# Performance work log

Hardware: AMD Instinct MI355X
Metric: run time of the kernel (lower is better)

## Reference

```python
import jax, jax.numpy as jnp
import numpy as np

N, CAMS = 1, 4
C1, C2, NH = 256, 256, 8
H1, H2, W2 = 128, 64, 400
H, W = 128, 128


def setup_inputs() -> dict:
    key = jax.random.key(0)
    ks = jax.random.split(key, 16)
    sc = 0.02
    th = jax.random.uniform(ks[3], (N, CAMS)) * 2.0 * np.pi
    c, s = jnp.cos(th), jnp.sin(th)
    z, o = jnp.zeros_like(c), jnp.ones_like(c)
    rots = jnp.stack([jnp.stack([c, -s, z], -1), jnp.stack([s, c, z], -1), jnp.stack([z, z, o], -1)], -2)
    return {
        "list_a": jax.random.normal(ks[0], (N, C1, H, W), jnp.float32),
        "list_b": jax.random.normal(ks[1], (N * CAMS, C2, H2, W2), jnp.float32),
        "fov_list": jax.random.uniform(ks[2], (N, CAMS)) * 0.5 + 1.0,
        "rots_list": rots.astype(jnp.float32),
        "trans_list": jax.random.normal(ks[4], (N, CAMS, 3), jnp.float32),
        "fxs": jax.random.uniform(ks[5], (N, CAMS)) * 100.0 + 500.0,
        "cxs": jax.random.uniform(ks[6], (N, CAMS)) * 20.0 + 390.0,
        "pos_a": jax.random.normal(ks[7], (1, H1, C1), jnp.float32),
        "pos_b": jax.random.normal(ks[8], (1, H2, C2), jnp.float32),
        "Wq": jax.random.normal(ks[9], (C1, C1), jnp.float32) * sc,
        "bq": jnp.zeros((C1,), jnp.float32),
        "Wk": jax.random.normal(ks[10], (C1, C2), jnp.float32) * sc,
        "bk": jnp.zeros((C1,), jnp.float32),
        "Wv": jax.random.normal(ks[11], (C1, C2), jnp.float32) * sc,
        "bv": jnp.zeros((C1,), jnp.float32),
        "in_w": jax.random.normal(ks[12], (3 * C1, C1), jnp.float32) * sc,
        "in_b": jnp.zeros((3 * C1,), jnp.float32),
        "out_w": jax.random.normal(ks[13], (C1, C1), jnp.float32) * sc,
        "out_b": jnp.zeros((C1,), jnp.float32),
    }


def _polar_coords(w1, h1, Hh, Ww, rots, fx, cx):
    # per-pixel viewing angles from intrinsics (original image width hard-coded 800)
    pi = jnp.arange(w1, dtype=jnp.float32)
    pw = 800.0 / w1
    ang = jnp.arctan((pi * pw + pw / 2.0 - cx) / fx)
    R90 = jnp.array([[0.0, 1.0], [-1.0, 0.0]], jnp.float32)
    rot = R90 @ rots[:2, :2].astype(jnp.float32)
    cr, sr = rot[0, 0], rot[1, 0]
    ca = cr * jnp.cos(ang) + sr * jnp.sin(ang)
    sa = -sr * jnp.cos(ang) + cr * jnp.sin(ang)
    cxp = jnp.float32(Ww // 2)
    cyp = jnp.float32(Hh // 2)
    rmax = jnp.sqrt(cxp ** 2 + cyp ** 2)
    radii = jnp.linspace(0.0, 1.0, h1).reshape(h1, 1) * rmax
    x = cxp + radii * ca  # [h1, w1]
    y = cyp - radii * sa
    return x, y


def _bilinear(img, x, y):
    # img [C,H,W]; x,y pixel coords [h1,w1]; grid_sample(align_corners=True) after clamping
    Hh, Ww = img.shape[1], img.shape[2]
    x = jnp.clip(x, 0.0, Ww - 1.0)
    y = jnp.clip(y, 0.0, Hh - 1.0)
    x0 = jnp.floor(x); y0 = jnp.floor(y)
    x1 = jnp.clip(x0 + 1.0, 0.0, Ww - 1.0)
    y1 = jnp.clip(y0 + 1.0, 0.0, Hh - 1.0)
    wx = x - x0; wy = y - y0
    x0i, x1i = x0.astype(jnp.int32), x1.astype(jnp.int32)
    y0i, y1i = y0.astype(jnp.int32), y1.astype(jnp.int32)
    v00 = img[:, y0i, x0i]; v01 = img[:, y0i, x1i]
    v10 = img[:, y1i, x0i]; v11 = img[:, y1i, x1i]
    return v00 * (1 - wx) * (1 - wy) + v01 * wx * (1 - wy) + v10 * (1 - wx) * wy + v11 * wx * wy


def _mha(q, k, v, in_w, in_b, out_w, out_b, nh):
    E = q.shape[-1]
    dh = E // nh
    qq = q @ in_w[:E].T + in_b[:E]
    kk = k @ in_w[E:2 * E].T + in_b[E:2 * E]
    vv = v @ in_w[2 * E:].T + in_b[2 * E:]
    B, Lq, _ = q.shape
    Lk = k.shape[1]
    qq = qq.reshape(B, Lq, nh, dh)
    kk = kk.reshape(B, Lk, nh, dh)
    vv = vv.reshape(B, Lk, nh, dh)
    att = jnp.einsum('bqhd,bkhd->bhqk', qq, kk) / jnp.sqrt(jnp.float32(dh))
    p = jax.nn.softmax(att, axis=-1)
    o = jnp.einsum('bhqk,bkhd->bqhd', p, vv).reshape(B, Lq, E)
    return o @ out_w.T + out_b


def _forward(list_a, list_b, rots_list, fxs, cxs, pos_a, pos_b,
             Wq, bq, Wk, bk, Wv, bv, in_w, in_b, out_w, out_b):
    outs = []
    for i in range(list_a.shape[0]):
        a = list_a[i]
        C1_, h1, Wb = a.shape
        Hb = h1
        enh = None
        for j in (0, 3):  # cameras 1 and 2 are skipped by the original `continue`
            b = list_b[i * CAMS + j]
            C2_, h2, w2 = b.shape
            x, y = _polar_coords(w2, h1, a.shape[1], a.shape[2], rots_list[i, j], fxs[i, j], cxs[i, j])
            a_rect = _bilinear(a, x, y)                     # [C1, h1, w2]
            a_seq = jnp.transpose(a_rect, (2, 1, 0)) + pos_a  # [w2, h1, C1]
            b_seq = jnp.transpose(b, (2, 1, 0)) + pos_b       # [w2, h2, C2]
            q = a_seq @ Wq.T + bq
            k = b_seq @ Wk.T + bk
            v = b_seq @ Wv.T + bv
            o = _mha(q, k, v, in_w, in_b, out_w, out_b, NH)
            a_enh = jnp.transpose(o, (2, 1, 0))              # [C1, h1, w2]
            # scatter-add restore with nearest-pixel indices
            xi = jnp.clip(jnp.round(x), 0, a.shape[2] - 1).astype(jnp.int32)
            yi = jnp.clip(jnp.round(y), 0, a.shape[1] - 1).astype(jnp.int32)
            idx = (yi * a.shape[2] + xi).reshape(-1)
            vals = a_enh.reshape(C1_, -1)
            rest = jnp.zeros((C1_, a.shape[1] * a.shape[2]), a.dtype).at[:, idx].add(vals)
            cnt = jnp.zeros((a.shape[1] * a.shape[2],), a.dtype).at[idx].add(1.0)
            cnt = jnp.where(cnt == 0, 1.0, cnt)
            enh = (rest / cnt).reshape(a.shape)
            a = a + enh
        outs.append(a + enh)  # original double-adds the last camera's enhancement
    return jnp.stack(outs)


def reference(list_a, list_b, fov_list, rots_list, trans_list, fxs, cxs, pos_a, pos_b,
              Wq, bq, Wk, bk, Wv, bv, in_w, in_b, out_w, out_b):
    # fov_list / trans_list are accepted but unused in the original math path
    return _forward(list_a, list_b, rots_list, fxs, cxs, pos_a, pos_b,
                    Wq, bq, Wk, bk, Wv, bv, in_w, in_b, out_w, out_b)
```

## Files before the change

kernel.cpp:

```cpp
#include <hip/hip_runtime.h>

#define PIX 16384
#define MS 51200
#define MB 25600

typedef __attribute__((ext_vector_type(8))) short short8;
typedef __attribute__((ext_vector_type(4))) float floatx4;

__device__ inline ushort f2b(float x) {
  uint u = __float_as_uint(x);
  return (ushort)((u + 0x7fffu + ((u >> 16) & 1u)) >> 16);
}
__device__ inline float b2f(ushort u) {
  return __uint_as_float(((uint)u) << 16);
}

__global__ __launch_bounds__(256) void coords_kernel(
    const float* __restrict__ rots, const float* __restrict__ fxs,
    const float* __restrict__ cxs,
    float* __restrict__ xarr, float* __restrict__ yarr,
    int* __restrict__ idxarr, float* __restrict__ cnt)
{
  int jz = blockIdx.y;
  int j = jz ? 3 : 0;
  int s = blockIdx.x * 256 + threadIdx.x;
  int h = s / 400;
  int w = s - h * 400;
  float fx = fxs[j], cx = cxs[j];
  const float* R = rots + j * 9;
  float cr = R[3];
  float sr = -R[0];
  float t = (2.0f * (float)w + 1.0f - cx) / fx;
  float inv = 1.0f / sqrtf(1.0f + t * t);
  float ca = (cr + sr * t) * inv;
  float sa = (cr * t - sr) * inv;
  float rad = ((float)h * (1.0f / 127.0f)) * 90.50966799187808f;
  float x = 64.0f + rad * ca;
  float y = 64.0f - rad * sa;
  xarr[jz * MS + s] = x;
  yarr[jz * MS + s] = y;
  int xi = (int)fminf(fmaxf(rintf(x), 0.0f), 127.0f);
  int yi = (int)fminf(fmaxf(rintf(y), 0.0f), 127.0f);
  int pix = yi * 128 + xi;
  idxarr[jz * MS + s] = pix;
  atomicAdd(&cnt[jz * PIX + pix], 1.0f);
}

__global__ __launch_bounds__(256) void prefix_kernel(
    const float* __restrict__ cntg, int* __restrict__ offsetsg)
{
  const float* cnt = cntg + blockIdx.x * PIX;
  int* offsets = offsetsg + blockIdx.x * PIX;
  __shared__ int sh[256];
  int t = threadIdx.x;
  int base = t * 64;
  const float4* cp = (const float4*)(cnt + base);
  int sum = 0;
#pragma unroll
  for (int i = 0; i < 16; ++i) {
    float4 v = cp[i];
    sum += (int)v.x + (int)v.y + (int)v.z + (int)v.w;
  }
  sh[t] = sum;
  __syncthreads();
  for (int d = 1; d < 256; d <<= 1) {
    int v = (t >= d) ? sh[t - d] : 0;
    __syncthreads();
    sh[t] += v;
    __syncthreads();
  }
  int run = sh[t] - sum;
  int4* op = (int4*)(offsets + base);
#pragma unroll
  for (int i = 0; i < 16; ++i) {
    float4 v = cp[i];
    int a0 = (int)v.x, a1 = (int)v.y, a2 = (int)v.z, a3 = (int)v.w;
    int4 o;
    o.x = run; o.y = run + a0; o.z = run + a0 + a1; o.w = run + a0 + a1 + a2;
    op[i] = o;
    run += a0 + a1 + a2 + a3;
  }
}

__global__ __launch_bounds__(256) void fill_kernel(
    const int* __restrict__ idxarr, const int* __restrict__ offsets,
    int* __restrict__ cursor, int* __restrict__ order, int* __restrict__ pixs)
{
  int jz = blockIdx.y;
  int s = blockIdx.x * 256 + threadIdx.x;
  int pix = idxarr[jz * MS + s];
  int pos = offsets[jz * PIX + pix] + atomicAdd(&cursor[jz * PIX + pix], 1);
  order[jz * MS + pos] = (s % 400) * 128 + (s / 400);
  pixs[jz * MS + pos] = pix;
}

__global__ __launch_bounds__(256) void transpose_kernel(
    const float* __restrict__ src, ushort* __restrict__ dst)
{
  __shared__ float tile[64][65];
  int p0 = blockIdx.x * 64;
  int c0 = blockIdx.y * 64;
  int t = threadIdx.x;
  int pr = (t & 15) * 4;
  int cr = t >> 4;
#pragma unroll
  for (int q = 0; q < 4; ++q) {
    int c = cr + q * 16;
    float4 v = *(const float4*)(src + (size_t)(c0 + c) * PIX + p0 + pr);
    tile[pr + 0][c] = v.x;
    tile[pr + 1][c] = v.y;
    tile[pr + 2][c] = v.z;
    tile[pr + 3][c] = v.w;
  }
  __syncthreads();
  int p = t >> 2;
  int ch = (t & 3) * 16;
  ushort tmp[16];
#pragma unroll
  for (int i = 0; i < 16; ++i) tmp[i] = f2b(tile[p][ch + i]);
  ushort* d = dst + (size_t)(p0 + p) * 256 + c0 + ch;
  *(uint4*)(d) = *(uint4*)tmp;
  *(uint4*)(d + 8) = *(uint4*)(tmp + 8);
}

__global__ __launch_bounds__(256) void misc_kernel(
    const float* __restrict__ out_w, ushort* __restrict__ out_wh,
    const float* __restrict__ in_w, const float* __restrict__ in_b,
    const float* __restrict__ bq, const float* __restrict__ bk,
    const float* __restrict__ bv, float* __restrict__ beff)
{
  if (blockIdx.x < 64) {
    int t = blockIdx.x * 256 + threadIdx.x;
    float4 v = ((const float4*)out_w)[t];
    ushort4 o;
    o.x = f2b(v.x); o.y = f2b(v.y); o.z = f2b(v.z); o.w = f2b(v.w);
    ((ushort4*)out_wh)[t] = o;
  } else {
    int z = blockIdx.x - 64;
    int f = threadIdx.x;
    const float* bsrc = (z == 0) ? bq : ((z == 1) ? bk : bv);
    const float* row = in_w + (size_t)(z * 256 + f) * 256;
    float acc = in_b[z * 256 + f];
    for (int e = 0; e < 256; ++e) acc += row[e] * bsrc[e];
    beff[z * 256 + f] = acc;
  }
}

#define LFP 264
__device__ __forceinline__ void sampleproj_body(
    ushort* lf, int bx,
    const ushort* __restrict__ aT, const float* __restrict__ xarr,
    const float* __restrict__ yarr, const ushort* __restrict__ Wh,
    const float* __restrict__ bias, ushort* __restrict__ qh)
{
  int s0 = bx * 64;
  int tid = threadIdx.x;
  int lane = tid & 63;
  int wave = tid >> 6;
  int col = lane & 15, quad = lane >> 4;
  int c0 = lane * 4;

#pragma unroll 4
  for (int i = 0; i < 16; ++i) {
    int sl = wave * 16 + i;
    int s = s0 + sl;
    float x = fminf(fmaxf(xarr[s], 0.0f), 127.0f);
    float y = fminf(fmaxf(yarr[s], 0.0f), 127.0f);
    float x0f = floorf(x), y0f = floorf(y);
    int x0 = (int)x0f, y0 = (int)y0f;
    int x1 = min(x0 + 1, 127), y1 = min(y0 + 1, 127);
    float wx = x - x0f, wy = y - y0f;
    float w00 = (1.0f - wx) * (1.0f - wy);
    float w01 = wx * (1.0f - wy);
    float w10 = (1.0f - wx) * wy;
    float w11 = wx * wy;
    ushort4 v00 = *(const ushort4*)(aT + (size_t)(y0 * 128 + x0) * 256 + c0);
    ushort4 v01 = *(const ushort4*)(aT + (size_t)(y0 * 128 + x1) * 256 + c0);
    ushort4 v10 = *(const ushort4*)(aT + (size_t)(y1 * 128 + x0) * 256 + c0);
    ushort4 v11 = *(const ushort4*)(aT + (size_t)(y1 * 128 + x1) * 256 + c0);
    ushort4 o;
    o.x = f2b(w00 * b2f(v00.x) + w01 * b2f(v01.x) + w10 * b2f(v10.x) + w11 * b2f(v11.x));
    o.y = f2b(w00 * b2f(v00.y) + w01 * b2f(v01.y) + w10 * b2f(v10.y) + w11 * b2f(v11.y));
    o.z = f2b(w00 * b2f(v00.z) + w01 * b2f(v01.z) + w10 * b2f(v10.z) + w11 * b2f(v11.z));
    o.w = f2b(w00 * b2f(v00.w) + w01 * b2f(v01.w) + w10 * b2f(v10.w) + w11 * b2f(v11.w));
    *(ushort4*)&lf[sl * LFP + c0] = o;
  }
  __syncthreads();

  int fw = wave * 64;
  floatx4 acc[4][4];
#pragma unroll
  for (int i = 0; i < 4; ++i)
#pragma unroll
    for (int jx = 0; jx < 4; ++jx) acc[i][jx] = (floatx4){0.f, 0.f, 0.f, 0.f};

  for (int kb = 0; kb < 256; kb += 32) {
    short8 aop[4], bop[4];
#pragma unroll
    for (int tf = 0; tf < 4; ++tf)
      aop[tf] = *(const short8*)(Wh + (size_t)(fw + tf * 16 + col) * 256 + kb + quad * 8);
#pragma unroll
    for (int ts = 0; ts < 4; ++ts)
      bop[ts] = *(const short8*)&lf[(ts * 16 + col) * LFP + kb + quad * 8];
#pragma unroll
    for (int ts = 0; ts < 4; ++ts)
#pragma unroll
      for (int tf = 0; tf < 4; ++tf)
        acc[ts][tf] = __builtin_amdgcn_mfma_f32_16x16x32_bf16(
            aop[tf], bop[ts], acc[ts][tf], 0, 0, 0);
  }
#pragma unroll
  for (int ts = 0; ts < 4; ++ts) {
    int s = s0 + ts * 16 + col;
    int h = s / 400;
    int w = s - h * 400;
    size_t obase = (size_t)(w * 128 + h) * 256;
#pragma unroll
    for (int tf = 0; tf < 4; ++tf) {
      int f = fw + tf * 16 + quad * 4;
      float4 bv = *(const float4*)(bias + h * 256 + f);
      ushort4 ov;
      ov.x = f2b(acc[ts][tf][0] + bv.x);
      ov.y = f2b(acc[ts][tf][1] + bv.y);
      ov.z = f2b(acc[ts][tf][2] + bv.z);
      ov.w = f2b(acc[ts][tf][3] + bv.w);
      *(ushort4*)(qh + obase + f) = ov;
    }
  }
}

__device__ __forceinline__ void projKV_body(
    ushort* lb, int bx,
    const float* __restrict__ bsrc,
    const ushort* __restrict__ WhK, const ushort* __restrict__ WhV,
    const float* __restrict__ biasK, const float* __restrict__ biasV,
    ushort* __restrict__ kh, ushort* __restrict__ vh)
{
  int m0 = bx * 64;
  int tid = threadIdx.x;
  int lane = tid & 63;
  int wave = tid >> 6;
  int col = lane & 15, quad = lane >> 4;
  int fw = wave * 64;

  int pr = (tid & 15) * 4;
  int cb = tid >> 4;
#pragma unroll 4
  for (int q = 0; q < 16; ++q) {
    int c = cb + q * 16;
    float4 v = *(const float4*)(bsrc + (size_t)c * MB + m0 + pr);
    lb[(pr + 0) * LFP + c] = f2b(v.x);
    lb[(pr + 1) * LFP + c] = f2b(v.y);
    lb[(pr + 2) * LFP + c] = f2b(v.z);
    lb[(pr + 3) * LFP + c] = f2b(v.w);
  }
  __syncthreads();

  for (int z = 0; z < 2; ++z) {
    const ushort* Wh = z ? WhV : WhK;
    const float* bias = z ? biasV : biasK;
    ushort* out = z ? vh : kh;
    floatx4 acc[4][4];
#pragma unroll
    for (int i = 0; i < 4; ++i)
#pragma unroll
      for (int jx = 0; jx < 4; ++jx) acc[i][jx] = (floatx4){0.f, 0.f, 0.f, 0.f};

    for (int kb = 0; kb < 256; kb += 32) {
      short8 bop[4], aop[4];
#pragma unroll
      for (int ts = 0; ts < 4; ++ts)
        bop[ts] = *(const short8*)&lb[(ts * 16 + col) * LFP + kb + quad * 8];
#pragma unroll
      for (int tf = 0; tf < 4; ++tf)
        aop[tf] = *(const short8*)(Wh + (size_t)(fw + tf * 16 + col) * 256 + kb + quad * 8);
#pragma unroll
      for (int ts = 0; ts < 4; ++ts)
#pragma unroll
        for (int tf = 0; tf < 4; ++tf)
          acc[ts][tf] = __builtin_amdgcn_mfma_f32_16x16x32_bf16(
              aop[tf], bop[ts], acc[ts][tf], 0, 0, 0);
    }
#pragma unroll
    for (int ts = 0; ts < 4; ++ts) {
      int m = m0 + ts * 16 + col;
      int h = m / 400;
      int w = m - h * 400;
      size_t obase = (size_t)(w * 64 + h) * 256;
#pragma unroll
      for (int tf = 0; tf < 4; ++tf) {
        int f = fw + tf * 16 + quad * 4;
        float4 bv = *(const float4*)(bias + h * 256 + f);
        ushort4 ov;
        ov.x = f2b(acc[ts][tf][0] + bv.x);
        ov.y = f2b(acc[ts][tf][1] + bv.y);
        ov.z = f2b(acc[ts][tf][2] + bv.z);
        ov.w = f2b(acc[ts][tf][3] + bv.w);
        *(ushort4*)(out + obase + f) = ov;
      }
    }
  }
}

__global__ __launch_bounds__(256, 3) void proj_kernel(
    const ushort* __restrict__ aT, const float* __restrict__ xarr,
    const float* __restrict__ yarr, const ushort* __restrict__ weffh,
    const float* __restrict__ qpos, ushort* __restrict__ qh,
    const float* __restrict__ bsrc,
    const float* __restrict__ kpos, const float* __restrict__ vpos,
    ushort* __restrict__ kh, ushort* __restrict__ vh)
{
  __shared__ ushort lf[64 * LFP];
  if (blockIdx.x < 400)
    projKV_body(lf, blockIdx.x, bsrc, weffh + 65536, weffh + 131072,
                kpos, vpos, kh, vh);
  else
    sampleproj_body(lf, blockIdx.x - 400, aT, xarr, yarr, weffh, qpos, qh);
}

#define VP 72
#define PP 72
__global__ __launch_bounds__(256) void attn_mfma_kernel(
    const ushort* __restrict__ qh, const ushort* __restrict__ kh,
    const ushort* __restrict__ vh, ushort* __restrict__ obuf)
{
  __shared__ ushort lV[4][32 * VP];
  __shared__ ushort lP[4][16 * PP];
  int b = blockIdx.x;
  int hg = blockIdx.y & 1;
  int qb = blockIdx.y >> 1;
  int wave = threadIdx.x >> 6;
  int lane = threadIdx.x & 63;
  int head = hg * 4 + wave;
  int col = lane & 15, quad = lane >> 4;
  ushort* Vw = lV[wave];
  ushort* Pw = lP[wave];

  short8 bk0 = *(const short8*)(kh + ((size_t)(b * 64 +  0 + col)) * 256 + head * 32 + quad * 8);
  short8 bk1 = *(const short8*)(kh + ((size_t)(b * 64 + 16 + col)) * 256 + head * 32 + quad * 8);
  short8 bk2 = *(const short8*)(kh + ((size_t)(b * 64 + 32 + col)) * 256 + head * 32 + quad * 8);
  short8 bk3 = *(const short8*)(kh + ((size_t)(b * 64 + 48 + col)) * 256 + head * 32 + quad * 8);

  {
    const ushort* vsrc = vh + ((size_t)(b * 64 + lane)) * 256 + head * 32;
    ushort vr[32];
    *(uint4*)(vr) = *(const uint4*)(vsrc);
    *(uint4*)(vr + 8) = *(const uint4*)(vsrc + 8);
    *(uint4*)(vr + 16) = *(const uint4*)(vsrc + 16);
    *(uint4*)(vr + 24) = *(const uint4*)(vsrc + 24);
#pragma unroll
    for (int d = 0; d < 32; ++d) Vw[d * VP + lane] = vr[d];
  }
  short8 vA0 = *(const short8*)(Vw + (col) * VP + 0 * 32 + quad * 8);
  short8 vB0 = *(const short8*)(Vw + (16 + col) * VP + 0 * 32 + quad * 8);
  short8 vA1 = *(const short8*)(Vw + (col) * VP + 1 * 32 + quad * 8);
  short8 vB1 = *(const short8*)(Vw + (16 + col) * VP + 1 * 32 + quad * 8);

  const float scl = 0.17677669529663687f;
  for (int qt = qb * 4; qt < qb * 4 + 4; ++qt) {
    short8 aq = *(const short8*)(qh +
        ((size_t)(b * 128 + qt * 16 + col)) * 256 + head * 32 + quad * 8);
    floatx4 s0 = {0.f,0.f,0.f,0.f}, s1 = s0, s2 = s0, s3 = s0;
    s0 = __builtin_amdgcn_mfma_f32_16x16x32_bf16(aq, bk0, s0, 0, 0, 0);
    s1 = __builtin_amdgcn_mfma_f32_16x16x32_bf16(aq, bk1, s1, 0, 0, 0);
    s2 = __builtin_amdgcn_mfma_f32_16x16x32_bf16(aq, bk2, s2, 0, 0, 0);
    s3 = __builtin_amdgcn_mfma_f32_16x16x32_bf16(aq, bk3, s3, 0, 0, 0);
    float e[4][4], mr[4], sm[4];
#pragma unroll
    for (int r = 0; r < 4; ++r) {
      float v0 = s0[r] * scl, v1 = s1[r] * scl;
      float v2 = s2[r] * scl, v3 = s3[r] * scl;
      e[0][r] = v0; e[1][r] = v1; e[2][r] = v2; e[3][r] = v3;
      mr[r] = fmaxf(fmaxf(v0, v1), fmaxf(v2, v3));
    }
#pragma unroll
    for (int mask = 1; mask <= 8; mask <<= 1)
#pragma unroll
      for (int r = 0; r < 4; ++r)
        mr[r] = fmaxf(mr[r], __shfl_xor(mr[r], mask, 64));
#pragma unroll
    for (int r = 0; r < 4; ++r) {
      float acc = 0.f;
#pragma unroll
      for (int t = 0; t < 4; ++t) {
        float ev = __expf(e[t][r] - mr[r]);
        e[t][r] = ev;
        acc += ev;
      }
      sm[r] = acc;
    }
#pragma unroll
    for (int mask = 1; mask <= 8; mask <<= 1)
#pragma unroll
      for (int r = 0; r < 4; ++r)
        sm[r] += __shfl_xor(sm[r], mask, 64);
#pragma unroll
    for (int t = 0; t < 4; ++t)
#pragma unroll
      for (int r = 0; r < 4; ++r)
        Pw[(quad * 4 + r) * PP + t * 16 + col] = f2b(e[t][r]);
    floatx4 o0 = {0.f,0.f,0.f,0.f}, o1 = o0;
    {
      short8 ap0 = *(const short8*)(Pw + col * PP + 0 * 32 + quad * 8);
      o0 = __builtin_amdgcn_mfma_f32_16x16x32_bf16(ap0, vA0, o0, 0, 0, 0);
      o1 = __builtin_amdgcn_mfma_f32_16x16x32_bf16(ap0, vB0, o1, 0, 0, 0);
      short8 ap1 = *(const short8*)(Pw + col * PP + 1 * 32 + quad * 8);
      o0 = __builtin_amdgcn_mfma_f32_16x16x32_bf16(ap1, vA1, o0, 0, 0, 0);
      o1 = __builtin_amdgcn_mfma_f32_16x16x32_bf16(ap1, vB1, o1, 0, 0, 0);
    }
#pragma unroll
    for (int r = 0; r < 4; ++r) {
      float iv = 1.0f / sm[r];
      Pw[(quad * 4 + r) * PP + col] = f2b(o0[r] * iv);
      Pw[(quad * 4 + r) * PP + 16 + col] = f2b(o1[r] * iv);
    }
    int orow = lane >> 2, ochunk = lane & 3;
    uint4 ov = *(const uint4*)(Pw + orow * PP + ochunk * 8);
    *(uint4*)(obuf + (size_t)(b * 128 + qt * 16 + orow) * 256 + head * 32 + ochunk * 8) = ov;
  }
}

__global__ __launch_bounds__(256) void gemmN3_kernel(
    const float* __restrict__ pos_a, const float* __restrict__ pos_b,
    const float* __restrict__ weff, const float* __restrict__ beff,
    float* __restrict__ qpos, float* __restrict__ kpos, float* __restrict__ vpos)
{
  int z = blockIdx.z;
  if (z > 0 && blockIdx.x > 0) return;
  const float* A = (z == 0) ? pos_a : pos_b;
  const float* Wt = weff + (size_t)z * 65536;
  const float* biasf = beff + z * 256;
  float* Cout = (z == 0) ? qpos : ((z == 1) ? kpos : vpos);
  __shared__ float As[64][17];
  __shared__ float Ws[16][65];
  int m0 = blockIdx.x * 64;
  int n0 = blockIdx.y * 64;
  int tid = threadIdx.x;
  int tx = tid & 15, ty = tid >> 4;
  float acc[4][4] = {};
  for (int k0 = 0; k0 < 256; k0 += 16) {
    {
      int m = tid >> 2;
      int kq = (tid & 3) << 2;
      float4 v = *(const float4*)(A + (size_t)(m0 + m) * 256 + k0 + kq);
      As[m][kq + 0] = v.x; As[m][kq + 1] = v.y;
      As[m][kq + 2] = v.z; As[m][kq + 3] = v.w;
    }
    {
      int f = tid >> 2;
      int kq = (tid & 3) << 2;
      float4 v = *(const float4*)(Wt + (size_t)(n0 + f) * 256 + k0 + kq);
      Ws[kq + 0][f] = v.x; Ws[kq + 1][f] = v.y;
      Ws[kq + 2][f] = v.z; Ws[kq + 3][f] = v.w;
    }
    __syncthreads();
#pragma unroll
    for (int kk = 0; kk < 16; ++kk) {
      float a[4], b[4];
#pragma unroll
      for (int i = 0; i < 4; ++i) a[i] = As[ty * 4 + i][kk];
#pragma unroll
      for (int jj = 0; jj < 4; ++jj) b[jj] = Ws[kk][tx * 4 + jj];
#pragma unroll
      for (int i = 0; i < 4; ++i)
#pragma unroll
        for (int jj = 0; jj < 4; ++jj) acc[i][jj] += a[i] * b[jj];
    }
    __syncthreads();
  }
#pragma unroll
  for (int i = 0; i < 4; ++i) {
    int m = m0 + ty * 4 + i;
    int f = n0 + tx * 4;
    float4 bv = *(const float4*)(biasf + f);
    float4 ov;
    ov.x = acc[i][0] + bv.x; ov.y = acc[i][1] + bv.y;
    ov.z = acc[i][2] + bv.z; ov.w = acc[i][3] + bv.w;
    *(float4*)(Cout + (size_t)m * 256 + f) = ov;
  }
}

__global__ __launch_bounds__(256) void gemm_ab_kernel(
    const float* __restrict__ in_w, const float* __restrict__ Wq,
    const float* __restrict__ Wk, const float* __restrict__ Wv,
    float* __restrict__ weff, ushort* __restrict__ weffh)
{
  int z = blockIdx.z;
  const float* A = in_w + (size_t)z * 65536;
  const float* B = (z == 0) ? Wq : ((z == 1) ? Wk : Wv);
  float* C = weff + (size_t)z * 65536;
  ushort* Ch = weffh + (size_t)z * 65536;
  __shared__ float As[64][17];
  __shared__ float Bs[16][64];
  int m0 = blockIdx.x * 64;
  int n0 = blockIdx.y * 64;
  int tid = threadIdx.x;
  int tx = tid & 15, ty = tid >> 4;
  float acc[4][4] = {};
  for (int k0 = 0; k0 < 256; k0 += 16) {
    {
      int m = tid >> 2;
      int kq = (tid & 3) << 2;
      float4 v = *(const float4*)(A + (size_t)(m0 + m) * 256 + k0 + kq);
      As[m][kq + 0] = v.x; As[m][kq + 1] = v.y;
      As[m][kq + 2] = v.z; As[m][kq + 3] = v.w;
    }
    {
      int k = tid >> 4;
      int nq = (tid & 15) << 2;
      float4 v = *(const float4*)(B + (size_t)(k0 + k) * 256 + n0 + nq);
      *(float4*)(&Bs[k][nq]) = v;
    }
    __syncthreads();
#pragma unroll
    for (int kk = 0; kk < 16; ++kk) {
      float a[4], b[4];
#pragma unroll
      for (int i = 0; i < 4; ++i) a[i] = As[ty * 4 + i][kk];
#pragma unroll
      for (int jj = 0; jj < 4; ++jj) b[jj] = Bs[kk][tx * 4 + jj];
#pragma unroll
      for (int i = 0; i < 4; ++i)
#pragma unroll
        for (int jj = 0; jj < 4; ++jj) acc[i][jj] += a[i] * b[jj];
    }
    __syncthreads();
  }
#pragma unroll
  for (int i = 0; i < 4; ++i) {
    int m = m0 + ty * 4 + i;
    *(float4*)(C + (size_t)m * 256 + n0 + tx * 4) = *(float4*)&acc[i][0];
    ushort4 hv;
    hv.x = f2b(acc[i][0]); hv.y = f2b(acc[i][1]);
    hv.z = f2b(acc[i][2]); hv.w = f2b(acc[i][3]);
    *(ushort4*)(Ch + (size_t)m * 256 + n0 + tx * 4) = hv;
  }
}

#define CH 64
__global__ __launch_bounds__(256) void segred_kernel(
    const ushort* __restrict__ obuf, const int* __restrict__ order,
    const int* __restrict__ pixs, float* __restrict__ osum)
{
  __shared__ int lm[CH];
  __shared__ int lp[CH + 2];
  int s0 = blockIdx.x * CH;
  int t = threadIdx.x;
  if (t < CH) {
    lm[t] = order[s0 + t];
    lp[t + 1] = pixs[s0 + t];
  } else if (t == CH) {
    lp[0] = (s0 > 0) ? pixs[s0 - 1] : -1;
  } else if (t == CH + 1) {
    lp[CH + 1] = (s0 + CH < MS) ? pixs[s0 + CH] : -2;
  }
  __syncthreads();
  int c = t;
  float va[8];
#pragma unroll
  for (int k = 0; k < 8; ++k)
    va[k] = b2f(obuf[(size_t)lm[k] * 256 + c]);
  float acc = 0.0f;
  int runBegin = 0;
#pragma unroll
  for (int i = 0; i < CH; ++i) {
    float v = va[i & 7];
    if (i + 8 < CH) va[i & 7] = b2f(obuf[(size_t)lm[i + 8] * 256 + c]);
    acc += v;
    int p = lp[i + 1];
    bool last = (i == CH - 1);
    if (last || p != lp[i + 2]) {
      bool pBeg = (runBegin == 0) && (p == lp[0]);
      bool pEnd = last && (p == lp[CH + 1]);
      float* dst = osum + (size_t)p * 256 + c;
      if (pBeg || pEnd) atomicAdd(dst, acc);
      else *dst = acc;
      acc = 0.0f;
      runBegin = i + 1;
    }
  }
}

__global__ __launch_bounds__(256) void outproj_update_kernel(
    const float* __restrict__ osum, const ushort* __restrict__ out_wh,
    const float* __restrict__ asrc, float* __restrict__ adst,
    const float* __restrict__ cnt, const float* __restrict__ out_b,
    float scale, ushort* __restrict__ aTout, int writeAT)
{
  int p0 = blockIdx.x * 32;
  int lane = threadIdx.x & 63;
  int wave = threadIdx.x >> 6;
  int col = lane & 15, quad = lane >> 4;
  int fw = wave * 64;
  floatx4 acc[2][4];
#pragma unroll
  for (int i = 0; i < 2; ++i)
#pragma unroll
    for (int jx = 0; jx < 4; ++jx) acc[i][jx] = (floatx4){0.f, 0.f, 0.f, 0.f};

  for (int kb = 0; kb < 256; kb += 32) {
    short8 aop[4], bop[2];
#pragma unroll
    for (int tf = 0; tf < 4; ++tf)
      aop[tf] = *(const short8*)(out_wh +
          (size_t)(fw + tf * 16 + col) * 256 + kb + quad * 8);
#pragma unroll
    for (int ts = 0; ts < 2; ++ts) {
      const float* brow = osum + (size_t)(p0 + ts * 16 + col) * 256 + kb + quad * 8;
      float4 f0 = *(const float4*)brow;
      float4 f1 = *(const float4*)(brow + 4);
      short8 bv;
      bv[0] = (short)f2b(f0.x); bv[1] = (short)f2b(f0.y);
      bv[2] = (short)f2b(f0.z); bv[3] = (short)f2b(f0.w);
      bv[4] = (short)f2b(f1.x); bv[5] = (short)f2b(f1.y);
      bv[6] = (short)f2b(f1.z); bv[7] = (short)f2b(f1.w);
      bop[ts] = bv;
    }
#pragma unroll
    for (int ts = 0; ts < 2; ++ts)
#pragma unroll
      for (int tf = 0; tf < 4; ++tf)
        acc[ts][tf] = __builtin_amdgcn_mfma_f32_16x16x32_bf16(
            aop[tf], bop[ts], acc[ts][tf], 0, 0, 0);
  }
#pragma unroll
  for (int ts = 0; ts < 2; ++ts) {
    int p = p0 + ts * 16 + col;
    float cn = cnt[p];
    float rs = scale / fmaxf(cn, 1.0f);
#pragma unroll
    for (int tf = 0; tf < 4; ++tf) {
      int f = fw + tf * 16 + quad * 4;
      float4 ob = *(const float4*)(out_b + f);
      float r0 = asrc[(size_t)(f + 0) * PIX + p] + (acc[ts][tf][0] + cn * ob.x) * rs;
      float r1 = asrc[(size_t)(f + 1) * PIX + p] + (acc[ts][tf][1] + cn * ob.y) * rs;
      float r2 = asrc[(size_t)(f + 2) * PIX + p] + (acc[ts][tf][2] + cn * ob.z) * rs;
      float r3 = asrc[(size_t)(f + 3) * PIX + p] + (acc[ts][tf][3] + cn * ob.w) * rs;
      adst[(size_t)(f + 0) * PIX + p] = r0;
      adst[(size_t)(f + 1) * PIX + p] = r1;
      adst[(size_t)(f + 2) * PIX + p] = r2;
      adst[(size_t)(f + 3) * PIX + p] = r3;
      if (writeAT) {
        ushort4 hv;
        hv.x = f2b(r0); hv.y = f2b(r1); hv.z = f2b(r2); hv.w = f2b(r3);
        *(ushort4*)(aTout + (size_t)p * 256 + f) = hv;
      }
    }
  }
}

extern "C" void kernel_launch(void* const* d_in, const int* in_sizes, int n_in,
                              void* d_out, int out_size, void* d_ws, size_t ws_size,
                              hipStream_t stream) {
  const float* list_a = (const float*)d_in[0];
  const float* list_b = (const float*)d_in[1];
  const float* rots   = (const float*)d_in[3];
  const float* fxs    = (const float*)d_in[5];
  const float* cxs    = (const float*)d_in[6];
  const float* pos_a  = (const float*)d_in[7];
  const float* pos_b  = (const float*)d_in[8];
  const float* Wq     = (const float*)d_in[9];
  const float* bq     = (const float*)d_in[10];
  const float* Wk     = (const float*)d_in[11];
  const float* bk     = (const float*)d_in[12];
  const float* Wv     = (const float*)d_in[13];
  const float* bv     = (const float*)d_in[14];
  const float* in_w   = (const float*)d_in[15];
  const float* in_b   = (const float*)d_in[16];
  const float* out_w  = (const float*)d_in[17];
  const float* out_b  = (const float*)d_in[18];

  float* ws      = (float*)d_ws;
  float* weff    = ws;
  float* beff    = weff + 196608;
  float* qpos    = beff + 768;
  float* kpos    = qpos + 32768;
  float* vpos    = kpos + 16384;
  float* a_cur   = vpos + 16384;
  float* xarr    = a_cur + 4194304;
  float* yarr    = xarr + 102400;
  int*   idxarr  = (int*)(yarr + 102400);
  int*   offs    = idxarr + 102400;
  int*   order   = offs + 32768;
  int*   pixs    = order + 102400;
  float* cnt     = (float*)(pixs + 102400);
  int*   cursor  = (int*)(cnt + 32768);
  float* osum    = (float*)(cursor + 32768);
  ushort* weffh  = (ushort*)(osum + 4194304);
  ushort* out_wh = weffh + 196608;
  ushort* obufh  = out_wh + 65536;
  ushort* qh     = obufh + 13107200;
  ushort* kh     = qh + 13107200;
  ushort* vh     = kh + 6553600;
  ushort* aT     = vh + 6553600;

  gemm_ab_kernel<<<dim3(4, 4, 3), 256, 0, stream>>>(in_w, Wq, Wk, Wv, weff, weffh);
  misc_kernel<<<67, 256, 0, stream>>>(out_w, out_wh, in_w, in_b, bq, bk, bv, beff);
  gemmN3_kernel<<<dim3(2, 4, 3), 256, 0, stream>>>(pos_a, pos_b, weff, beff,
                                                   qpos, kpos, vpos);
  hipMemsetAsync(cnt, 0, (size_t)(32768 + 32768) * sizeof(float), stream);
  coords_kernel<<<dim3(200, 2), 256, 0, stream>>>(rots, fxs, cxs, xarr, yarr, idxarr, cnt);
  prefix_kernel<<<2, 256, 0, stream>>>(cnt, offs);
  fill_kernel<<<dim3(200, 2), 256, 0, stream>>>(idxarr, offs, cursor, order, pixs);

  for (int jj = 0; jj < 2; ++jj) {
    int j = jj ? 3 : 0;
    const float* asrc = jj ? a_cur : list_a;
    hipMemsetAsync(osum, 0, (size_t)4194304 * sizeof(float), stream);
    if (jj == 0)
      transpose_kernel<<<dim3(256, 4), 256, 0, stream>>>(list_a, aT);
    proj_kernel<<<1200, 256, 0, stream>>>(aT, xarr + jj * MS, yarr + jj * MS,
                                          weffh, qpos, qh,
                                          list_b + (size_t)j * 6553600,
                                          kpos, vpos, kh, vh);
    attn_mfma_kernel<<<dim3(400, 4), 256, 0, stream>>>(qh, kh, vh, obufh);
    segred_kernel<<<800, 256, 0, stream>>>(obufh, order + jj * MS, pixs + jj * MS, osum);
    outproj_update_kernel<<<512, 256, 0, stream>>>(osum, out_wh, asrc,
                                                   jj ? (float*)d_out : a_cur,
                                                   cnt + jj * PIX, out_b,
                                                   jj ? 2.0f : 1.0f,
                                                   aT, jj == 0 ? 1 : 0);
  }
}
```

Before: 545.1 us.

## Store Q/K/V in natural row order and vectorize bf16 staging stores

The Q and K/V projection epilogues now write each output row at its natural (h*400+w) position instead of transposing to (w, h) order. The attention kernel changes its addressing to match, so its per-column reads become strided by 400 rows. This trades contiguous reads in attention for contiguous writes in the projections. Separately, the K/V staging loop loads four channels per thread and writes packed ushort4 values to LDS instead of single 16-bit stores.

After: 549.5 us. About the same (+0.8%).

```diff
diff --git a/kernel.cpp b/kernel.cpp
--- a/kernel.cpp
+++ b/kernel.cpp
@@ -213,8 +213,7 @@
   for (int ts = 0; ts < 4; ++ts) {
     int s = s0 + ts * 16 + col;
     int h = s / 400;
-    int w = s - h * 400;
-    size_t obase = (size_t)(w * 128 + h) * 256;
+    size_t obase = (size_t)s * 256;
 #pragma unroll
     for (int tf = 0; tf < 4; ++tf) {
       int f = fw + tf * 16 + quad * 4;
@@ -243,16 +242,23 @@
   int col = lane & 15, quad = lane >> 4;
   int fw = wave * 64;
 
-  int pr = (tid & 15) * 4;
-  int cb = tid >> 4;
-#pragma unroll 4
-  for (int q = 0; q < 16; ++q) {
-    int c = cb + q * 16;
-    float4 v = *(const float4*)(bsrc + (size_t)c * MB + m0 + pr);
-    lb[(pr + 0) * LFP + c] = f2b(v.x);
-    lb[(pr + 1) * LFP + c] = f2b(v.y);
-    lb[(pr + 2) * LFP + c] = f2b(v.z);
-    lb[(pr + 3) * LFP + c] = f2b(v.w);
+  int m4 = (tid & 15) * 4;
+  int c4 = (tid >> 4) * 4;
+#pragma unroll
+  for (int cq = 0; cq < 4; ++cq) {
+    int c = c4 + cq * 64;
+    float4 v0 = *(const float4*)(bsrc + (size_t)(c + 0) * MB + m0 + m4);
+    float4 v1 = *(const float4*)(bsrc + (size_t)(c + 1) * MB + m0 + m4);
+    float4 v2 = *(const float4*)(bsrc + (size_t)(c + 2) * MB + m0 + m4);
+    float4 v3 = *(const float4*)(bsrc + (size_t)(c + 3) * MB + m0 + m4);
+    ushort4 w0; w0.x = f2b(v0.x); w0.y = f2b(v1.x); w0.z = f2b(v2.x); w0.w = f2b(v3.x);
+    ushort4 w1; w1.x = f2b(v0.y); w1.y = f2b(v1.y); w1.z = f2b(v2.y); w1.w = f2b(v3.y);
+    ushort4 w2; w2.x = f2b(v0.z); w2.y = f2b(v1.z); w2.z = f2b(v2.z); w2.w = f2b(v3.z);
+    ushort4 w3; w3.x = f2b(v0.w); w3.y = f2b(v1.w); w3.z = f2b(v2.w); w3.w = f2b(v3.w);
+    *(ushort4*)&lb[(m4 + 0) * LFP + c] = w0;
+    *(ushort4*)&lb[(m4 + 1) * LFP + c] = w1;
+    *(ushort4*)&lb[(m4 + 2) * LFP + c] = w2;
+    *(ushort4*)&lb[(m4 + 3) * LFP + c] = w3;
   }
   __syncthreads();
 
@@ -285,8 +291,7 @@
     for (int ts = 0; ts < 4; ++ts) {
       int m = m0 + ts * 16 + col;
       int h = m / 400;
-      int w = m - h * 400;
-      size_t obase = (size_t)(w * 64 + h) * 256;
+      size_t obase = (size_t)m * 256;
 #pragma unroll
       for (int tf = 0; tf < 4; ++tf) {
         int f = fw + tf * 16 + quad * 4;
@@ -336,13 +341,13 @@
   ushort* Vw = lV[wave];
   ushort* Pw = lP[wave];
 
-  short8 bk0 = *(const short8*)(kh + ((size_t)(b * 64 +  0 + col)) * 256 + head * 32 + quad * 8);
-  short8 bk1 = *(const short8*)(kh + ((size_t)(b * 64 + 16 + col)) * 256 + head * 32 + quad * 8);
-  short8 bk2 = *(const short8*)(kh + ((size_t)(b * 64 + 32 + col)) * 256 + head * 32 + quad * 8);
-  short8 bk3 = *(const short8*)(kh + ((size_t)(b * 64 + 48 + col)) * 256 + head * 32 + quad * 8);
+  short8 bk0 = *(const short8*)(kh + ((size_t)(( 0 + col) * 400 + b)) * 256 + head * 32 + quad * 8);
+  short8 bk1 = *(const short8*)(kh + ((size_t)((16 + col) * 400 + b)) * 256 + head * 32 + quad * 8);
+  short8 bk2 = *(const short8*)(kh + ((size_t)((32 + col) * 400 + b)) * 256 + head * 32 + quad * 8);
+  short8 bk3 = *(const short8*)(kh + ((size_t)((48 + col) * 400 + b)) * 256 + head * 32 + quad * 8);
 
   {
-    const ushort* vsrc = vh + ((size_t)(b * 64 + lane)) * 256 + head * 32;
+    const ushort* vsrc = vh + ((size_t)(lane * 400 + b)) * 256 + head * 32;
     ushort vr[32];
     *(uint4*)(vr) = *(const uint4*)(vsrc);
     *(uint4*)(vr + 8) = *(const uint4*)(vsrc + 8);
@@ -359,7 +364,7 @@
   const float scl = 0.17677669529663687f;
   for (int qt = qb * 4; qt < qb * 4 + 4; ++qt) {
     short8 aq = *(const short8*)(qh +
-        ((size_t)(b * 128 + qt * 16 + col)) * 256 + head * 32 + quad * 8);
+        ((size_t)((qt * 16 + col) * 400 + b)) * 256 + head * 32 + quad * 8);
     floatx4 s0 = {0.f,0.f,0.f,0.f}, s1 = s0, s2 = s0, s3 = s0;
     s0 = __builtin_amdgcn_mfma_f32_16x16x32_bf16(aq, bk0, s0, 0, 0, 0);
     s1 = __builtin_amdgcn_mfma_f32_16x16x32_bf16(aq, bk1, s1, 0, 0, 0);
```
